# Kernel tuning notes

Measured on AMD Instinct MI355X. Metric: run time of the kernel, lower is better.

The kernel has to match this reference:

```python
import jax, jax.numpy as jnp
import numpy as np

ALPHA = 0.2  # LeakyReLU negative slope
NEG_INF = jnp.float32(-9e15)


def setup_inputs() -> dict:
    key = jax.random.key(0)
    k1, k2, k3, k4, k5, k6 = jax.random.split(key, 6)
    B, N, F_in, F_out = 8, 2048, 256, 64
    h = jax.random.normal(k1, (B, N, F_in), dtype=jnp.float32)
    adj = jax.random.randint(k2, (B, N, N), 0, 2, dtype=jnp.int32)
    level = jax.random.uniform(k3, (B, N), dtype=jnp.float32)
    node_type = jax.random.uniform(k4, (B, N, N), dtype=jnp.float32)
    W = jax.random.normal(k5, (F_in, F_out), dtype=jnp.float32) * 1.414 / np.sqrt(F_in)
    a = jax.random.normal(k6, (2 * F_out, 1), dtype=jnp.float32) * 1.414 / np.sqrt(2 * F_out)
    return {"h": h, "adj": adj, "level": level, "node_type": node_type, "W": W, "a": a}


def reference(h, adj, level, node_type, W, a):
    # h: [B,N,Fin], adj/node_type: [B,N,N], level: [B,N], W: [Fin,Fout], a: [2*Fout,1]
    F_out = W.shape[1]
    Wh = jnp.einsum('bnf,fo->bno', h, W)  # [B,N,Fout]
    # Additive attention decomposed: e[b,i,j] = a1.Wh_i + a2.Wh_j (no O(N^2*2F) tensor)
    a1 = a[:F_out, 0]
    a2 = a[F_out:, 0]
    f1 = Wh @ a1  # [B,N]
    f2 = Wh @ a2  # [B,N]
    e = jax.nn.leaky_relu(f1[:, :, None] + f2[:, None, :], negative_slope=ALPHA)  # [B,N,N]
    # gat_our=True path: node_type scales scores, level scales Wh
    e = e * node_type
    Wh = Wh * level[:, :, None]
    attention = jnp.where(adj > 0, e, NEG_INF)
    attention = jax.nn.softmax(attention, axis=1)  # faithful: original softmax over dim=1
    # dropout p=0 / eval mode -> identity
    h_prime = jnp.einsum('bij,bjo->bio', attention, Wh)  # [B,N,Fout]
    return jax.nn.relu(h_prime)  # concat=True
```

## Files before the change

kernel.cpp:

```cpp
#include <hip/hip_runtime.h>

#define BB 8
#define NN 2048
#define FIN 256
#define FO 64

typedef short short8_t __attribute__((ext_vector_type(8)));
typedef float float4_t __attribute__((ext_vector_type(4)));

__device__ __forceinline__ unsigned short f2bf(float x) {
  unsigned int u = __float_as_uint(x);
  unsigned int r = (u + 0x7fffu + ((u >> 16) & 1u)) >> 16;
  return (unsigned short)r;
}

#define GLD16(gp, lp)                                                          \
  __builtin_amdgcn_global_load_lds(                                            \
      (const __attribute__((address_space(1))) void*)(gp),                     \
      (__attribute__((address_space(3))) void*)(lp), 16, 0, 0)

__global__ __launch_bounds__(256) void k0_zero(float* __restrict__ scol) {
  scol[blockIdx.x * 256 + threadIdx.x] = 0.0f;
}

__global__ __launch_bounds__(256) void k1_gemm(
    const float* __restrict__ h,
    const float* __restrict__ level,
    const float* __restrict__ W,
    const float* __restrict__ a,
    float* __restrict__ V, float* __restrict__ f1, float* __restrict__ f2)
{
  __shared__ float wlds[128 * 64];
  __shared__ float hs[16 * 260];
  __shared__ float parts1[16 * 17];
  __shared__ float parts2[16 * 17];
  int t = threadIdx.x;
  int b = blockIdx.x >> 7;
  int i0 = (blockIdx.x & 127) * 16;

  {
    int r_ld = t >> 4, f0 = (t & 15) * 16;
    const float* hp = h + (size_t)(b * NN + i0 + r_ld) * FIN + f0;
    float4 x0 = *(const float4*)(hp);
    float4 x1 = *(const float4*)(hp + 4);
    float4 x2 = *(const float4*)(hp + 8);
    float4 x3 = *(const float4*)(hp + 12);
    float* hd = &hs[r_ld * 260 + f0];
    *(float4*)(hd + 0) = x0; *(float4*)(hd + 4) = x1;
    *(float4*)(hd + 8) = x2; *(float4*)(hd + 12) = x3;
  }

  int r = t >> 4;
  int c4 = (t & 15) * 4;
  float4 acc = {0, 0, 0, 0};

  #pragma unroll
  for (int half = 0; half < 2; ++half) {
    __syncthreads();
    #pragma unroll
    for (int q = 0; q < 8; ++q) {
      int idx = q * 1024 + t * 4;
      *(float4*)&wlds[idx] = *(const float4*)&W[half * 8192 + idx];
    }
    __syncthreads();
    for (int f = 0; f < 128; f += 8) {
      float4 hv0 = *(const float4*)&hs[r * 260 + half * 128 + f];
      float4 hv1 = *(const float4*)&hs[r * 260 + half * 128 + f + 4];
      float hvv[8] = {hv0.x, hv0.y, hv0.z, hv0.w, hv1.x, hv1.y, hv1.z, hv1.w};
      #pragma unroll
      for (int k = 0; k < 8; ++k) {
        float4 wv = *(const float4*)&wlds[(f + k) * 64 + c4];
        acc.x += hvv[k] * wv.x; acc.y += hvv[k] * wv.y;
        acc.z += hvv[k] * wv.z; acc.w += hvv[k] * wv.w;
      }
    }
  }

  float p1 = acc.x * a[c4] + acc.y * a[c4 + 1] + acc.z * a[c4 + 2] + acc.w * a[c4 + 3];
  float p2 = acc.x * a[64 + c4] + acc.y * a[64 + c4 + 1] +
             acc.z * a[64 + c4 + 2] + acc.w * a[64 + c4 + 3];
  parts1[r * 17 + (t & 15)] = p1;
  parts2[r * 17 + (t & 15)] = p2;
  __syncthreads();
  if (t < 16) {
    float s1 = 0.f, s2 = 0.f;
    #pragma unroll
    for (int g = 0; g < 16; ++g) { s1 += parts1[t * 17 + g]; s2 += parts2[t * 17 + g]; }
    f1[b * NN + i0 + t] = s1;
    f2[b * NN + i0 + t] = s2;
  }

  float lv = level[b * NN + i0 + r];
  float4 vv = {acc.x * lv, acc.y * lv, acc.z * lv, acc.w * lv};
  *(float4*)&V[(size_t)(b * NN + i0 + r) * FO + c4] = vv;
}

template <int STORE_U>
__global__ __launch_bounds__(256) void k2a_stats(
    const int* __restrict__ adj,
    const float* __restrict__ ntp,
    const float* __restrict__ f1,
    const float* __restrict__ f2,
    unsigned short* __restrict__ u_bf,
    unsigned char* __restrict__ bits,
    float* __restrict__ scol)
{
  __shared__ int ladj[2][8 * 256];
  __shared__ float lnt[2][8 * 256];
  __shared__ float red[4 * 264];
  int t = threadIdx.x;
  int b = blockIdx.x >> 8;
  int i0 = (blockIdx.x & 255) * 8;
  int w = t >> 6, l = t & 63;
  size_t rbase = (size_t)(b * NN + i0);
  int r0 = 2 * w;

  auto stage = [&](int buf, int c) {
    #pragma unroll
    for (int r = 0; r < 2; ++r) {
      int row = r0 + r;
      const int* ga = adj + (rbase + row) * NN + c * 256 + l * 4;
      const float* gn = ntp + (rbase + row) * NN + c * 256 + l * 4;
      GLD16(ga, &ladj[buf][row * 256]);
      GLD16(gn, &lnt[buf][row * 256]);
    }
  };

  stage(0, 0);

  float f1v0 = f1[rbase + r0];
  float f1v1 = f1[rbase + r0 + 1];
  float f2all[32];
  #pragma unroll
  for (int c = 0; c < 8; ++c)
    #pragma unroll
    for (int k = 0; k < 4; ++k)
      f2all[c * 4 + k] = f2[b * NN + c * 256 + 64 * k + l];

  for (int c = 0; c < 8; ++c) {
    int cur = c & 1;
    __syncthreads();

    float acc4[4] = {0, 0, 0, 0};
    #pragma unroll
    for (int r = 0; r < 2; ++r) {
      int row = r0 + r;
      float f1v = r ? f1v1 : f1v0;
      #pragma unroll
      for (int k = 0; k < 4; ++k) {
        int av = ladj[cur][row * 256 + 64 * k + l];
        float nv = lnt[cur][row * 256 + 64 * k + l];
        float x = f1v + f2all[c * 4 + k];
        x = fmaxf(x, 0.2f * x);
        bool m = av > 0;
        float u = m ? __expf(x * nv) : 0.0f;
        acc4[k] += u;
        if (STORE_U) {
          u_bf[(rbase + row) * NN + c * 256 + 64 * k + l] = f2bf(u);
        } else {
          unsigned long long bal = __ballot(m);
          if (l == 0)
            *(unsigned long long*)&bits[(rbase + row) * (NN / 8) + c * 32 + k * 8] = bal;
        }
      }
    }
    #pragma unroll
    for (int k = 0; k < 4; ++k) red[w * 264 + 64 * k + l] = acc4[k];
    __syncthreads();

    if (c < 7) stage(cur ^ 1, c + 1);

    float s = red[0 * 264 + t % 256] + red[1 * 264 + t] + red[2 * 264 + t] + red[3 * 264 + t];
    atomicAdd(&scol[b * NN + c * 256 + t], s);
  }
}

__global__ __launch_bounds__(256) void k2b_pack(
    const float* __restrict__ V,
    const float* __restrict__ scol,
    unsigned short* __restrict__ vf)
{
  int t = threadIdx.x;
  int b = blockIdx.x >> 6;
  int kk = blockIdx.x & 63;
  int ng = t >> 6;
  int l = t & 63;
  int jb = kk * 32 + ((l >> 4) * 8);
  int o = ng * 16 + (l & 15);
  unsigned int pk[4];
  #pragma unroll
  for (int p = 0; p < 4; ++p) {
    int jr0 = jb + 2 * p, jr1 = jb + 2 * p + 1;
    float s0 = scol[b * NN + jr0];
    float s1 = scol[b * NN + jr1];
    float i0 = (s0 > 0.f) ? (1.0f / s0) : 0.0f;
    float i1 = (s1 > 0.f) ? (1.0f / s1) : 0.0f;
    float v0 = V[(size_t)(b * NN + jr0) * FO + o] * i0;
    float v1 = V[(size_t)(b * NN + jr1) * FO + o] * i1;
    pk[p] = (unsigned int)f2bf(v0) | ((unsigned int)f2bf(v1) << 16);
  }
  *(uint4*)(vf + (size_t)(((b * 64 + kk) * 4 + ng) * 64 + l) * 8) =
      make_uint4(pk[0], pk[1], pk[2], pk[3]);
}

__global__ __launch_bounds__(256) void k3_agg_u(
    const unsigned short* __restrict__ u_bf,
    const unsigned short* __restrict__ vf,
    float* __restrict__ outp)
{
  __shared__ float red[4 * 16 * 68];
  int t = threadIdx.x;
  int b = blockIdx.x >> 7;
  int i0 = (blockIdx.x & 127) * 16;
  int w = t >> 6, l = t & 63;
  int col = l & 15, quad = l >> 4;
  const unsigned short* urow = u_bf + (size_t)(b * NN + i0 + col) * NN + quad * 8;
  const unsigned short* vbase = vf + (size_t)(b * 64) * 2048 + l * 8;

  short8_t Aall[16];
  #pragma unroll
  for (int s = 0; s < 16; ++s)
    Aall[s] = *(const short8_t*)(urow + (size_t)(w * 16 + s) * 32);

  const unsigned short* vb0 = vbase + (size_t)(w * 16) * 2048;
  short8_t c0 = *(const short8_t*)(vb0);
  short8_t c1 = *(const short8_t*)(vb0 + 512);
  short8_t c2 = *(const short8_t*)(vb0 + 1024);
  short8_t c3 = *(const short8_t*)(vb0 + 1536);

  float4_t acc0 = {0, 0, 0, 0}, acc1 = {0, 0, 0, 0}, acc2 = {0, 0, 0, 0}, acc3 = {0, 0, 0, 0};

  #pragma unroll
  for (int s = 0; s < 16; ++s) {
    short8_t n0, n1, n2, n3;
    if (s < 15) {
      const unsigned short* vn = vbase + (size_t)(w * 16 + s + 1) * 2048;
      n0 = *(const short8_t*)(vn);
      n1 = *(const short8_t*)(vn + 512);
      n2 = *(const short8_t*)(vn + 1024);
      n3 = *(const short8_t*)(vn + 1536);
    }
    acc0 = __builtin_amdgcn_mfma_f32_16x16x32_bf16(Aall[s], c0, acc0, 0, 0, 0);
    acc1 = __builtin_amdgcn_mfma_f32_16x16x32_bf16(Aall[s], c1, acc1, 0, 0, 0);
    acc2 = __builtin_amdgcn_mfma_f32_16x16x32_bf16(Aall[s], c2, acc2, 0, 0, 0);
    acc3 = __builtin_amdgcn_mfma_f32_16x16x32_bf16(Aall[s], c3, acc3, 0, 0, 0);
    if (s < 15) { c0 = n0; c1 = n1; c2 = n2; c3 = n3; }
  }

  #pragma unroll
  for (int r = 0; r < 4; ++r) {
    int rowi = quad * 4 + r;
    red[w * 1088 + rowi * 68 + 0 + col] = acc0[r];
    red[w * 1088 + rowi * 68 + 16 + col] = acc1[r];
    red[w * 1088 + rowi * 68 + 32 + col] = acc2[r];
    red[w * 1088 + rowi * 68 + 48 + col] = acc3[r];
  }
  __syncthreads();

  int row = t >> 4, o4 = (t & 15) * 4;
  const float* rp = &red[row * 68 + o4];
  float4 s0 = *(const float4*)(rp);
  float4 s1 = *(const float4*)(rp + 1088);
  float4 s2 = *(const float4*)(rp + 2176);
  float4 s3 = *(const float4*)(rp + 3264);
  float4 o;
  o.x = fmaxf(s0.x + s1.x + s2.x + s3.x, 0.0f);
  o.y = fmaxf(s0.y + s1.y + s2.y + s3.y, 0.0f);
  o.z = fmaxf(s0.z + s1.z + s2.z + s3.z, 0.0f);
  o.w = fmaxf(s0.w + s1.w + s2.w + s3.w, 0.0f);
  *(float4*)&outp[(size_t)(b * NN + i0 + row) * FO + o4] = o;
}

__global__ __launch_bounds__(256) void k3_agg_b(
    const float* __restrict__ ntp,
    const unsigned char* __restrict__ bits,
    const float* __restrict__ f1,
    const float* __restrict__ f2,
    const unsigned short* __restrict__ vf,
    float* __restrict__ outp)
{
  __shared__ float red[4 * 16 * 68];
  int t = threadIdx.x;
  int b = blockIdx.x >> 7;
  int i0 = (blockIdx.x & 127) * 16;
  int w = t >> 6, l = t & 63;
  int col = l & 15, quad = l >> 4;
  int gi = b * NN + i0 + col;
  float f1v = f1[gi];
  const float* ntrow = ntp + (size_t)gi * NN;
  const unsigned char* brow = bits + (size_t)gi * (NN / 8);
  float4_t acc0 = {0, 0, 0, 0}, acc1 = {0, 0, 0, 0}, acc2 = {0, 0, 0, 0}, acc3 = {0, 0, 0, 0};

  for (int s = 0; s < 16; ++s) {
    int kk = w * 16 + s;
    int jq = kk * 32 + quad * 8;
    unsigned int m8 = brow[jq >> 3];
    float4 n0 = *(const float4*)(ntrow + jq);
    float4 n1 = *(const float4*)(ntrow + jq + 4);
    float4 g0 = *(const float4*)(f2 + b * NN + jq);
    float4 g1 = *(const float4*)(f2 + b * NN + jq + 4);
    float f2v[8] = {g0.x, g0.y, g0.z, g0.w, g1.x, g1.y, g1.z, g1.w};
    float ntf[8] = {n0.x, n0.y, n0.z, n0.w, n1.x, n1.y, n1.z, n1.w};
    union { unsigned int u[4]; short8_t v; } A;
    #pragma unroll
    for (int p = 0; p < 4; ++p) {
      int e0 = 2 * p, e1 = 2 * p + 1;
      float x0 = f1v + f2v[e0]; x0 = fmaxf(x0, 0.2f * x0);
      float u0 = ((m8 >> e0) & 1u) ? __expf(x0 * ntf[e0]) : 0.0f;
      float x1 = f1v + f2v[e1]; x1 = fmaxf(x1, 0.2f * x1);
      float u1 = ((m8 >> e1) & 1u) ? __expf(x1 * ntf[e1]) : 0.0f;
      A.u[p] = (unsigned int)f2bf(u0) | ((unsigned int)f2bf(u1) << 16);
    }
    const unsigned short* vb = vf + (size_t)(b * 64 + kk) * 2048 + l * 8;
    short8_t bf0 = *(const short8_t*)(vb);
    short8_t bf1 = *(const short8_t*)(vb + 512);
    short8_t bf2 = *(const short8_t*)(vb + 1024);
    short8_t bf3 = *(const short8_t*)(vb + 1536);
    acc0 = __builtin_amdgcn_mfma_f32_16x16x32_bf16(A.v, bf0, acc0, 0, 0, 0);
    acc1 = __builtin_amdgcn_mfma_f32_16x16x32_bf16(A.v, bf1, acc1, 0, 0, 0);
    acc2 = __builtin_amdgcn_mfma_f32_16x16x32_bf16(A.v, bf2, acc2, 0, 0, 0);
    acc3 = __builtin_amdgcn_mfma_f32_16x16x32_bf16(A.v, bf3, acc3, 0, 0, 0);
  }

  #pragma unroll
  for (int r = 0; r < 4; ++r) {
    int rowi = quad * 4 + r;
    red[w * 1088 + rowi * 68 + 0 + col] = acc0[r];
    red[w * 1088 + rowi * 68 + 16 + col] = acc1[r];
    red[w * 1088 + rowi * 68 + 32 + col] = acc2[r];
    red[w * 1088 + rowi * 68 + 48 + col] = acc3[r];
  }
  __syncthreads();

  int row = t >> 4, o4 = (t & 15) * 4;
  const float* rp = &red[row * 68 + o4];
  float4 s0 = *(const float4*)(rp);
  float4 s1 = *(const float4*)(rp + 1088);
  float4 s2 = *(const float4*)(rp + 2176);
  float4 s3 = *(const float4*)(rp + 3264);
  float4 o;
  o.x = fmaxf(s0.x + s1.x + s2.x + s3.x, 0.0f);
  o.y = fmaxf(s0.y + s1.y + s2.y + s3.y, 0.0f);
  o.z = fmaxf(s0.z + s1.z + s2.z + s3.z, 0.0f);
  o.w = fmaxf(s0.w + s1.w + s2.w + s3.w, 0.0f);
  *(float4*)&outp[(size_t)(b * NN + i0 + row) * FO + o4] = o;
}

extern "C" void kernel_launch(void* const* d_in, const int* in_sizes, int n_in,
                              void* d_out, int out_size, void* d_ws, size_t ws_size,
                              hipStream_t stream) {
  const float* h = (const float*)d_in[0];
  const int* adj = (const int*)d_in[1];
  const float* level = (const float*)d_in[2];
  const float* ntm = (const float*)d_in[3];
  const float* W = (const float*)d_in[4];
  const float* a = (const float*)d_in[5];
  float* outp = (float*)d_out;

  float* V = (float*)d_ws;
  float* f1 = V + (size_t)BB * NN * FO;
  float* f2 = f1 + BB * NN;
  float* scol = f2 + BB * NN;
  unsigned short* vf = (unsigned short*)(scol + BB * NN);
  char* tail = (char*)(vf + (size_t)BB * NN * FO);
  size_t fixed = (size_t)(tail - (char*)d_ws);
  size_t need_u = fixed + (size_t)BB * NN * NN * 2;
  bool big = (ws_size >= need_u);

  k0_zero<<<64, 256, 0, stream>>>(scol);
  k1_gemm<<<1024, 256, 0, stream>>>(h, level, W, a, V, f1, f2);
  if (big) {
    unsigned short* u_bf = (unsigned short*)tail;
    k2a_stats<1><<<2048, 256, 0, stream>>>(adj, ntm, f1, f2, u_bf, nullptr, scol);
    k2b_pack<<<512, 256, 0, stream>>>(V, scol, vf);
    k3_agg_u<<<1024, 256, 0, stream>>>(u_bf, vf, outp);
  } else {
    unsigned char* bits = (unsigned char*)tail;
    k2a_stats<0><<<2048, 256, 0, stream>>>(adj, ntm, f1, f2, nullptr, bits, scol);
    k2b_pack<<<512, 256, 0, stream>>>(V, scol, vf);
    k3_agg_b<<<1024, 256, 0, stream>>>(ntm, bits, f1, f2, vf, outp);
  }
}
```

Measured before the change: 349.3 us.

## Tile stats kernel over 32 rows and store attention weights in MFMA fragment layout

The stats kernel now runs 512-thread blocks over 32 rows each. Column sums are accumulated in registers across two 16-row tiles, which replaces per-chunk LDS reductions with one final reduction and issues four times fewer atomics. The bf16 attention weights are written directly in the tiled layout the aggregation kernel's MFMA A-operand loads consume, so those loads become contiguous 16-byte per-lane reads. The separate zeroing kernel is folded into the GEMM kernel to save a launch. In exchange, the u_bf stores become more scattered 2-byte writes, and the larger blocks use more LDS per block, which may lower occupancy.

```diff
diff --git a/kernel.cpp b/kernel.cpp
--- a/kernel.cpp
+++ b/kernel.cpp
@@ -18,17 +18,14 @@
   __builtin_amdgcn_global_load_lds(                                            \
       (const __attribute__((address_space(1))) void*)(gp),                     \
       (__attribute__((address_space(3))) void*)(lp), 16, 0, 0)
-
-__global__ __launch_bounds__(256) void k0_zero(float* __restrict__ scol) {
-  scol[blockIdx.x * 256 + threadIdx.x] = 0.0f;
-}
 
 __global__ __launch_bounds__(256) void k1_gemm(
     const float* __restrict__ h,
     const float* __restrict__ level,
     const float* __restrict__ W,
     const float* __restrict__ a,
-    float* __restrict__ V, float* __restrict__ f1, float* __restrict__ f2)
+    float* __restrict__ V, float* __restrict__ f1, float* __restrict__ f2,
+    float* __restrict__ scol)
 {
   __shared__ float wlds[128 * 64];
   __shared__ float hs[16 * 260];
@@ -37,6 +34,8 @@
   int t = threadIdx.x;
   int b = blockIdx.x >> 7;
   int i0 = (blockIdx.x & 127) * 16;
+
+  if (blockIdx.x < 64) scol[blockIdx.x * 256 + t] = 0.0f;
 
   {
     int r_ld = t >> 4, f0 = (t & 15) * 16;
@@ -96,7 +95,7 @@
 }
 
 template <int STORE_U>
-__global__ __launch_bounds__(256) void k2a_stats(
+__global__ __launch_bounds__(512) void k2a_stats(
     const int* __restrict__ adj,
     const float* __restrict__ ntp,
     const float* __restrict__ f1,
@@ -105,74 +104,83 @@
     unsigned char* __restrict__ bits,
     float* __restrict__ scol)
 {
-  __shared__ int ladj[2][8 * 256];
-  __shared__ float lnt[2][8 * 256];
-  __shared__ float red[4 * 264];
-  int t = threadIdx.x;
-  int b = blockIdx.x >> 8;
-  int i0 = (blockIdx.x & 255) * 8;
+  __shared__ int ladj[2][16 * 256];
+  __shared__ float lnt[2][16 * 256];
+  __shared__ float red[2048];
+  int t = threadIdx.x;
+  int b = blockIdx.x >> 6;
+  int row0 = (blockIdx.x & 63) * 32;
   int w = t >> 6, l = t & 63;
-  size_t rbase = (size_t)(b * NN + i0);
-  int r0 = 2 * w;
-
-  auto stage = [&](int buf, int c) {
-    #pragma unroll
-    for (int r = 0; r < 2; ++r) {
-      int row = r0 + r;
-      const int* ga = adj + (rbase + row) * NN + c * 256 + l * 4;
-      const float* gn = ntp + (rbase + row) * NN + c * 256 + l * 4;
-      GLD16(ga, &ladj[buf][row * 256]);
-      GLD16(gn, &lnt[buf][row * 256]);
-    }
+  size_t base = (size_t)b * NN;
+
+  auto stage = [&](int buf, int s) {
+    int tile = s >> 3, c = s & 7;
+    int r0 = row0 + tile * 16 + 2 * w;
+    const int* ga = adj + (base + r0) * NN + c * 256 + l * 4;
+    const float* gn = ntp + (base + r0) * NN + c * 256 + l * 4;
+    GLD16(ga, &ladj[buf][(2 * w) * 256]);
+    GLD16(ga + NN, &ladj[buf][(2 * w + 1) * 256]);
+    GLD16(gn, &lnt[buf][(2 * w) * 256]);
+    GLD16(gn + NN, &lnt[buf][(2 * w + 1) * 256]);
   };
 
+  int jj = t & 255;
+  int rh = t >> 8;
+  int kk_in = jj >> 5;
+  int quad = (jj & 31) >> 3;
+  int e = jj & 7;
+
+  float accJ[8];
+  #pragma unroll
+  for (int c = 0; c < 8; ++c) accJ[c] = 0.f;
+  float f2v[8];
+  #pragma unroll
+  for (int c = 0; c < 8; ++c) f2v[c] = f2[base + c * 256 + jj];
+
   stage(0, 0);
-
-  float f1v0 = f1[rbase + r0];
-  float f1v1 = f1[rbase + r0 + 1];
-  float f2all[32];
-  #pragma unroll
-  for (int c = 0; c < 8; ++c)
-    #pragma unroll
-    for (int k = 0; k < 4; ++k)
-      f2all[c * 4 + k] = f2[b * NN + c * 256 + 64 * k + l];
-
-  for (int c = 0; c < 8; ++c) {
-    int cur = c & 1;
+  for (int s = 0; s < 16; ++s) {
+    int buf = s & 1;
     __syncthreads();
-
-    float acc4[4] = {0, 0, 0, 0};
-    #pragma unroll
-    for (int r = 0; r < 2; ++r) {
-      int row = r0 + r;
-      float f1v = r ? f1v1 : f1v0;
-      #pragma unroll
-      for (int k = 0; k < 4; ++k) {
-        int av = ladj[cur][row * 256 + 64 * k + l];
-        float nv = lnt[cur][row * 256 + 64 * k + l];
-        float x = f1v + f2all[c * 4 + k];
-        x = fmaxf(x, 0.2f * x);
-        bool m = av > 0;
-        float u = m ? __expf(x * nv) : 0.0f;
-        acc4[k] += u;
-        if (STORE_U) {
-          u_bf[(rbase + row) * NN + c * 256 + 64 * k + l] = f2bf(u);
-        } else {
-          unsigned long long bal = __ballot(m);
-          if (l == 0)
-            *(unsigned long long*)&bits[(rbase + row) * (NN / 8) + c * 32 + k * 8] = bal;
-        }
+    if (s < 15) stage(buf ^ 1, s + 1);
+    int tile = s >> 3, c = s & 7;
+    int it = (row0 >> 4) + tile;
+    size_t fbase = ((size_t)(b * 128 + it) * 64 + (c * 8 + kk_in)) * 512
+                   + quad * 128 + rh * 64 + e;
+    #pragma unroll
+    for (int q = 0; q < 8; ++q) {
+      int r = rh * 8 + q;
+      int av = ladj[buf][r * 256 + jj];
+      float nv = lnt[buf][r * 256 + jj];
+      float f1v = f1[base + row0 + tile * 16 + r];
+      float x = f1v + f2v[c];
+      x = fmaxf(x, 0.2f * x);
+      bool m = av > 0;
+      float u = m ? __expf(x * nv) : 0.0f;
+      accJ[c] += u;
+      if (STORE_U) {
+        u_bf[fbase + q * 8] = f2bf(u);
+      } else {
+        unsigned long long bal = __ballot(m);
+        if (l == 0)
+          *(unsigned long long*)&bits[(base + row0 + tile * 16 + r) * (NN / 8)
+                                      + c * 32 + (w & 3) * 8] = bal;
       }
     }
-    #pragma unroll
-    for (int k = 0; k < 4; ++k) red[w * 264 + 64 * k + l] = acc4[k];
-    __syncthreads();
-
-    if (c < 7) stage(cur ^ 1, c + 1);
-
-    float s = red[0 * 264 + t % 256] + red[1 * 264 + t] + red[2 * 264 + t] + red[3 * 264 + t];
-    atomicAdd(&scol[b * NN + c * 256 + t], s);
-  }
+  }
+
+  if (rh == 0) {
+    #pragma unroll
+    for (int c = 0; c < 8; ++c) red[c * 256 + jj] = accJ[c];
+  }
+  __syncthreads();
+  if (rh == 1) {
+    #pragma unroll
+    for (int c = 0; c < 8; ++c) red[c * 256 + jj] += accJ[c];
+  }
+  __syncthreads();
+  #pragma unroll
+  for (int q = 0; q < 4; ++q)
+    atomicAdd(&scol[base + q * 512 + t], red[q * 512 + t]);
 }
 
 __global__ __launch_bounds__(256) void k2b_pack(
@@ -211,16 +219,17 @@
   __shared__ float red[4 * 16 * 68];
   int t = threadIdx.x;
   int b = blockIdx.x >> 7;
-  int i0 = (blockIdx.x & 127) * 16;
+  int it = blockIdx.x & 127;
+  int i0 = it * 16;
   int w = t >> 6, l = t & 63;
   int col = l & 15, quad = l >> 4;
-  const unsigned short* urow = u_bf + (size_t)(b * NN + i0 + col) * NN + quad * 8;
+  const unsigned short* abase = u_bf + ((size_t)(b * 128 + it) * 64) * 512 + l * 8;
   const unsigned short* vbase = vf + (size_t)(b * 64) * 2048 + l * 8;
 
   short8_t Aall[16];
   #pragma unroll
   for (int s = 0; s < 16; ++s)
-    Aall[s] = *(const short8_t*)(urow + (size_t)(w * 16 + s) * 32);
+    Aall[s] = *(const short8_t*)(abase + (size_t)(w * 16 + s) * 512);
 
   const unsigned short* vb0 = vbase + (size_t)(w * 16) * 2048;
   short8_t c0 = *(const short8_t*)(vb0);
@@ -367,16 +376,15 @@
   size_t need_u = fixed + (size_t)BB * NN * NN * 2;
   bool big = (ws_size >= need_u);
 
-  k0_zero<<<64, 256, 0, stream>>>(scol);
-  k1_gemm<<<1024, 256, 0, stream>>>(h, level, W, a, V, f1, f2);
+  k1_gemm<<<1024, 256, 0, stream>>>(h, level, W, a, V, f1, f2, scol);
   if (big) {
     unsigned short* u_bf = (unsigned short*)tail;
-    k2a_stats<1><<<2048, 256, 0, stream>>>(adj, ntm, f1, f2, u_bf, nullptr, scol);
+    k2a_stats<1><<<512, 512, 0, stream>>>(adj, ntm, f1, f2, u_bf, nullptr, scol);
     k2b_pack<<<512, 256, 0, stream>>>(V, scol, vf);
     k3_agg_u<<<1024, 256, 0, stream>>>(u_bf, vf, outp);
   } else {
     unsigned char* bits = (unsigned char*)tail;
-    k2a_stats<0><<<2048, 256, 0, stream>>>(adj, ntm, f1, f2, nullptr, bits, scol);
+    k2a_stats<0><<<512, 512, 0, stream>>>(adj, ntm, f1, f2, nullptr, bits, scol);
     k2b_pack<<<512, 256, 0, stream>>>(V, scol, vf);
     k3_agg_b<<<1024, 256, 0, stream>>>(ntm, bits, f1, f2, vf, outp);
   }
```

New measurement: 346.6 us. Within noise of the previous version (-0.8%).
